# Kernel tuning notes

Hardware: AMD Instinct MI355X
Metric: run time of the kernel (lower is better)

Reference implementation:

```python
import jax, jax.numpy as jnp
import numpy as np

B, S, E, H = 8, 1024, 256, 8
HD = E // H
SCALE = HD ** -0.5
EPS = 1e-5


def setup_inputs() -> dict:
    key = jax.random.key(0)
    ks = jax.random.split(key, 12)
    n = lambda i, shape, sc=1.0: jax.random.normal(ks[i], shape, jnp.float32) * sc
    return {
        "x": n(0, (B, S, E)),
        "x2": n(1, (B, S, E)),
        "pde_qk": n(2, (S, S), 0.1),
        "in_proj_w": n(3, (3 * E, E), 0.03),
        "in_proj_b": jnp.zeros((3 * E,), jnp.float32),
        "out_w": n(4, (E, E), 0.03),
        "out_b": jnp.zeros((E,), jnp.float32),
        "gamma": jnp.ones((E,), jnp.float32),
        "beta": jnp.zeros((E,), jnp.float32),
        "gamma2": jnp.ones((E,), jnp.float32),
        "beta2": jnp.zeros((E,), jnp.float32),
        "bn_weight": jnp.zeros((), jnp.float32),
    }


def _mha(x, pde_qk, wi, bi, wo, bo):
    # qkv in one projection, as in _in_proj with qkv_same
    qkv = x @ wi.T + bi                       # [B,S,3E]
    q, k, v = jnp.split(qkv, 3, axis=-1)
    q = q * SCALE
    hd = lambda t: t.reshape(B, S, H, HD).transpose(0, 2, 1, 3)  # [B,H,S,HD]
    q, k, v = hd(q), hd(k), hd(v)
    # pairwise pde bias fused into scores (broadcast over batch/head)
    scores = jnp.einsum("bhsd,bhtd->bhst", q, k) + pde_qk        # [B,H,S,S]
    w = jax.nn.softmax(scores, axis=-1)
    a = jnp.einsum("bhst,bhtd->bhsd", w, v)
    a = a.transpose(0, 2, 1, 3).reshape(B, S, E)
    return a @ wo.T + bo


def _dual_bn(X, X2, gamma, beta, gamma2, beta2, bn_weight):
    # training branch: learned sigmoid gate mixes per-feature stats across domains
    w = (jax.nn.sigmoid(bn_weight) + 1.0) / 2.0
    m1 = X.mean(axis=(0, 1), keepdims=True)
    v1 = ((X - m1) ** 2).mean(axis=(0, 1), keepdims=True)
    m2 = X2.mean(axis=(0, 1), keepdims=True)
    v2 = ((X2 - m2) ** 2).mean(axis=(0, 1), keepdims=True)
    m_fa = w * m1 + (1 - w) * m2
    m_fb = w * m2 + (1 - w) * m1
    v_fa = w * v1 + (1 - w) * v2
    v_fb = w * v2 + (1 - w) * v1
    Y = gamma * ((X - m_fa) / jnp.sqrt(v_fa + EPS)) + beta
    Y2 = gamma2 * ((X2 - m_fb) / jnp.sqrt(v_fb + EPS)) + beta2
    return Y, Y2


def _mmd(src, tgt, kernel_mul=2.0, kernel_num=5):
    n = src.shape[0] + tgt.shape[0]
    total = jnp.concatenate([src, tgt], axis=0)        # [2B,E]
    d = ((total[None, :, :] - total[:, None, :]) ** 2).sum(-1)  # [2B,2B]
    # bandwidth uses .data (no grad) in torch -> stop_gradient
    bw = jax.lax.stop_gradient(d.sum()) / (n * n - n)
    bw = bw / (kernel_mul ** (kernel_num // 2))
    kern = sum(jnp.exp(-d / (bw * kernel_mul ** i)) for i in range(kernel_num))
    b = src.shape[0]
    XX, YY = kern[:b, :b], kern[b:, b:]
    XY, YX = kern[:b, b:], kern[b:, :b]
    return jnp.mean(XX + YY - XY - YX)


def reference(x, x2, pde_qk, in_proj_w, in_proj_b, out_w, out_b,
              gamma, beta, gamma2, beta2, bn_weight):
    Ya = _mha(x, pde_qk, in_proj_w, in_proj_b, out_w, out_b)
    Yb = _mha(x2, pde_qk, in_proj_w, in_proj_b, out_w, out_b)
    Y, Y2 = _dual_bn(Ya, Yb, gamma, beta, gamma2, beta2, bn_weight)
    # MMD alignment between temporally mean-pooled domain features
    loss = _mmd(Y.mean(axis=1), Y2.mean(axis=1))
    return Y, Y2, loss
```

## Files before the change

### kernel.cpp

```cpp
#include <hip/hip_runtime.h>
#include <hip/hip_bf16.h>

#define B_ 8
#define S_ 1024
#define E_ 256
#define H_ 8
#define HD_ 32
#define SCALE_ 0.17677669529663687f
#define LOG2E_ 1.44269504088896f
#define QSCALE_ (SCALE_ * LOG2E_)
#define EPS_ 1e-5f

typedef __attribute__((ext_vector_type(8))) short bf16x8;
typedef __attribute__((ext_vector_type(4))) short bf16x4;
typedef __attribute__((ext_vector_type(4))) float f32x4;

__device__ inline short f2bf(float f) {
    union { float f; unsigned u; } v; v.f = f;
    unsigned r = v.u + 0x7fff + ((v.u >> 16) & 1);
    return (short)(r >> 16);
}

__device__ inline unsigned packbf(float a, float b) {
    union { float f; unsigned u; } va, vb; va.f = a; vb.f = b;
    return ((va.u + 0x8000u) >> 16) | ((vb.u + 0x8000u) & 0xffff0000u);
}

__device__ inline int swz(int row, int kbyte) {
    return row * 512 + (kbyte ^ ((row & 7) << 4));
}

__global__ __launch_bounds__(256) void k_pde(
    const float* __restrict__ pde, short* __restrict__ out)
{
    int idx = blockIdx.x * 256 + threadIdx.x;
    int s = idx >> 10, t = idx & 1023;
    int dest = (s >> 4) * 16384 + (t >> 4) * 256
             + ((((t >> 2) & 3) << 4) | (s & 15)) * 4 + (t & 3);
    out[dest] = f2bf(pde[idx] * LOG2E_);
}

__global__ __launch_bounds__(256) void k_qkv(
    const float* __restrict__ x0, const float* __restrict__ x1,
    const float* __restrict__ w, const float* __restrict__ bias,
    short* __restrict__ qws, short* __restrict__ kws, short* __restrict__ vws)
{
    __shared__ alignas(16) short lA[64 * 256];
    __shared__ alignas(16) short lB[64 * 256];
    const int m0 = blockIdx.x * 64;
    const int n0 = blockIdx.y * 64;
    const int inp = blockIdx.z;
    const float* x = inp ? x1 : x0;
    const int tid = threadIdx.x;

    #pragma unroll
    for (int i = 0; i < 16; ++i) {
        int fid = tid + 256 * i;
        int r = fid >> 6, c4 = fid & 63;
        float4 vv = *reinterpret_cast<const float4*>(x + (long)(m0 + r) * 256 + c4 * 4);
        short4 sv; sv.x = f2bf(vv.x); sv.y = f2bf(vv.y); sv.z = f2bf(vv.z); sv.w = f2bf(vv.w);
        *reinterpret_cast<short4*>(reinterpret_cast<char*>(lA) + swz(r, c4 * 8)) = sv;
    }
    #pragma unroll
    for (int i = 0; i < 16; ++i) {
        int fid = tid + 256 * i;
        int r = fid >> 6, c4 = fid & 63;
        float4 vv = *reinterpret_cast<const float4*>(w + (long)(n0 + r) * 256 + c4 * 4);
        short4 sv; sv.x = f2bf(vv.x); sv.y = f2bf(vv.y); sv.z = f2bf(vv.z); sv.w = f2bf(vv.w);
        *reinterpret_cast<short4*>(reinterpret_cast<char*>(lB) + swz(r, c4 * 8)) = sv;
    }
    __syncthreads();

    const int wv = tid >> 6, ln = tid & 63;
    const int row16 = ln & 15, kg = ln >> 4;
    const int arow = wv * 16 + row16;
    f32x4 acc[4] = {};
    #pragma unroll
    for (int kc = 0; kc < 8; ++kc) {
        int kbyte = kc * 64 + kg * 16;
        bf16x8 af = *reinterpret_cast<const bf16x8*>(
            reinterpret_cast<char*>(lA) + swz(arow, kbyte));
        #pragma unroll
        for (int n = 0; n < 4; ++n) {
            int brow = n * 16 + row16;
            bf16x8 bfg = *reinterpret_cast<const bf16x8*>(
                reinterpret_cast<char*>(lB) + swz(brow, kbyte));
            acc[n] = __builtin_amdgcn_mfma_f32_16x16x32_bf16(af, bfg, acc[n], 0, 0, 0);
        }
    }
    #pragma unroll
    for (int n = 0; n < 4; ++n) {
        int o = n0 + n * 16 + row16;
        float bval = bias[o];
        int sect = o >> 8, e = o & 255, h = e >> 5, d = e & 31;
        #pragma unroll
        for (int r = 0; r < 4; ++r) {
            int grow = m0 + wv * 16 + kg * 4 + r;
            int b = grow >> 10, s = grow & 1023;
            float val = acc[n][r] + bval;
            long gi = (long)(inp * 64 + b * 8 + h) * 32768;
            if (sect == 0) {
                qws[gi + (s >> 4) * 512 + (((d >> 3) << 4) | (s & 15)) * 8 + (d & 7)]
                    = f2bf(val * QSCALE_);
            } else if (sect == 1) {
                kws[gi + (s >> 4) * 512 + (((d >> 3) << 4) | (s & 15)) * 8 + (d & 7)]
                    = f2bf(val);
            } else {
                vws[gi + (s >> 4) * 512 + (d >> 4) * 256
                       + ((((s >> 2) & 3) << 4) | (d & 15)) * 4 + (s & 3)]
                    = f2bf(val);
            }
        }
    }
}

__global__ __launch_bounds__(256) void k_attn(
    const short* __restrict__ qws, const short* __restrict__ kws,
    const short* __restrict__ vws, const short* __restrict__ pdef,
    short* __restrict__ aout)
{
    const int L = blockIdx.x;
    const int xcd = L & 7, kidx = L >> 3;
    const int qb = kidx >> 4;
    const int g  = xcd * 16 + (kidx & 15);
    const int inp = g >> 6, bh = g & 63, b = bh >> 3, h = bh & 7;
    const int tid = threadIdx.x, wv = tid >> 6, ln = tid & 63;
    const int row16 = ln & 15, kg = ln >> 4;
    const long gbase = (long)g * 32768;
    const int sb = qb * 4 + wv;

    bf16x8 qf = *reinterpret_cast<const bf16x8*>(qws + gbase + sb * 512 + ln * 8);
    const short* kp = kws + gbase + ln * 8;
    const short* vp = vws + gbase + ln * 4;
    const short* pp = pdef + (long)sb * 16384 + ln * 4;

    f32x4 acc0 = {}, acc1 = {};
    float lsum = 0.f;

    #pragma unroll 4
    for (int tb = 0; tb < 64; ++tb) {
        bf16x8 kf = *reinterpret_cast<const bf16x8*>(kp + tb * 512);
        short4 pb = *reinterpret_cast<const short4*>(pp + tb * 256);
        f32x4 c;
        c[0] = __uint_as_float((unsigned)(unsigned short)pb.x << 16);
        c[1] = __uint_as_float((unsigned)(unsigned short)pb.y << 16);
        c[2] = __uint_as_float((unsigned)(unsigned short)pb.z << 16);
        c[3] = __uint_as_float((unsigned)(unsigned short)pb.w << 16);
        f32x4 sv = __builtin_amdgcn_mfma_f32_16x16x32_bf16(kf, qf, c, 0, 0, 0);
        float p0 = exp2f(sv[0]), p1 = exp2f(sv[1]);
        float p2 = exp2f(sv[2]), p3 = exp2f(sv[3]);
        lsum += (p0 + p1) + (p2 + p3);
        union { unsigned u[2]; bf16x4 v; } pa;
        pa.u[0] = packbf(p0, p1);
        pa.u[1] = packbf(p2, p3);
        bf16x4 v0 = *reinterpret_cast<const bf16x4*>(vp + tb * 512);
        bf16x4 v1 = *reinterpret_cast<const bf16x4*>(vp + tb * 512 + 256);
        acc0 = __builtin_amdgcn_mfma_f32_16x16x16bf16_1k(pa.v, v0, acc0, 0, 0, 0);
        acc1 = __builtin_amdgcn_mfma_f32_16x16x16bf16_1k(pa.v, v1, acc1, 0, 0, 0);
    }

    lsum += __shfl_xor(lsum, 16);
    lsum += __shfl_xor(lsum, 32);
    float lq[4];
    #pragma unroll
    for (int r = 0; r < 4; ++r) lq[r] = __shfl(lsum, kg * 4 + r);

    #pragma unroll
    for (int c2 = 0; c2 < 2; ++c2) {
        int e = h * 32 + c2 * 16 + row16;
        #pragma unroll
        for (int r = 0; r < 4; ++r) {
            int s = qb * 64 + wv * 16 + kg * 4 + r;
            float val = (c2 ? acc1[r] : acc0[r]) / lq[r];
            aout[((long)inp * 8192 + b * 1024 + s) * 256 + e] = f2bf(val);
        }
    }
}

__global__ __launch_bounds__(256) void k_outproj(
    const short* __restrict__ a, const float* __restrict__ w,
    const float* __restrict__ bias, float* __restrict__ yout,
    float* __restrict__ chsum, float* __restrict__ chsq,
    float* __restrict__ bsum)
{
    __shared__ alignas(16) short lA[64 * 256];
    __shared__ alignas(16) short lB[64 * 256];
    const int m0 = blockIdx.x * 64;
    const int n0 = blockIdx.y * 64;
    const int inp = blockIdx.z;
    const int tid = threadIdx.x;
    const short* asrc = a + (long)inp * 8192 * 256;

    #pragma unroll
    for (int i = 0; i < 16; ++i) {
        int fid = tid + 256 * i;
        int r = fid >> 6, c4 = fid & 63;
        short4 sv = *reinterpret_cast<const short4*>(asrc + (long)(m0 + r) * 256 + c4 * 4);
        *reinterpret_cast<short4*>(reinterpret_cast<char*>(lA) + swz(r, c4 * 8)) = sv;
    }
    #pragma unroll
    for (int i = 0; i < 16; ++i) {
        int fid = tid + 256 * i;
        int r = fid >> 6, c4 = fid & 63;
        float4 vv = *reinterpret_cast<const float4*>(w + (long)(n0 + r) * 256 + c4 * 4);
        short4 sv; sv.x = f2bf(vv.x); sv.y = f2bf(vv.y); sv.z = f2bf(vv.z); sv.w = f2bf(vv.w);
        *reinterpret_cast<short4*>(reinterpret_cast<char*>(lB) + swz(r, c4 * 8)) = sv;
    }
    __syncthreads();

    const int wv = tid >> 6, ln = tid & 63;
    const int row16 = ln & 15, kg = ln >> 4;
    const int arow = wv * 16 + row16;
    f32x4 acc[4] = {};
    #pragma unroll
    for (int kc = 0; kc < 8; ++kc) {
        int kbyte = kc * 64 + kg * 16;
        bf16x8 af = *reinterpret_cast<const bf16x8*>(
            reinterpret_cast<char*>(lA) + swz(arow, kbyte));
        #pragma unroll
        for (int n = 0; n < 4; ++n) {
            int brow = n * 16 + row16;
            bf16x8 bfg = *reinterpret_cast<const bf16x8*>(
                reinterpret_cast<char*>(lB) + swz(brow, kbyte));
            acc[n] = __builtin_amdgcn_mfma_f32_16x16x32_bf16(af, bfg, acc[n], 0, 0, 0);
        }
    }
    #pragma unroll
    for (int n = 0; n < 4; ++n) {
        int o = n0 + n * 16 + row16;
        float bv = bias[o];
        float sum = 0.f, sq = 0.f;
        #pragma unroll
        for (int r = 0; r < 4; ++r) {
            long grow = m0 + wv * 16 + kg * 4 + r;
            float val = acc[n][r] + bv;
            yout[(long)inp * 2097152 + grow * 256 + o] = val;
            sum += val; sq += val * val;
        }
        sum += __shfl_xor(sum, 16); sum += __shfl_xor(sum, 32);
        sq  += __shfl_xor(sq, 16);  sq  += __shfl_xor(sq, 32);
        if (kg == 0) {
            atomicAdd(&chsum[inp * 256 + o], sum);
            atomicAdd(&chsq[inp * 256 + o], sq);
            int b = m0 >> 10;
            atomicAdd(&bsum[(inp * 8 + b) * 256 + o], sum);
        }
    }
}

__global__ __launch_bounds__(256) void k_finalize(
    const float* __restrict__ chsum, const float* __restrict__ chsq,
    const float* __restrict__ bsum, const float* __restrict__ gamma,
    const float* __restrict__ beta, const float* __restrict__ gamma2,
    const float* __restrict__ beta2, const float* __restrict__ bnw,
    float* __restrict__ params, float* __restrict__ loss_out)
{
    __shared__ float tot[16][257];
    __shared__ float red[8];
    const int tid = threadIdx.x;
    const float w = (1.f / (1.f + __expf(-bnw[0])) + 1.f) * 0.5f;
    const int e = tid;
    float m1 = chsum[e] * (1.f / 8192.f);
    float v1 = chsq[e] * (1.f / 8192.f) - m1 * m1;
    float m2 = chsum[256 + e] * (1.f / 8192.f);
    float v2 = chsq[256 + e] * (1.f / 8192.f) - m2 * m2;
    float mfa = w * m1 + (1.f - w) * m2, mfb = w * m2 + (1.f - w) * m1;
    float vfa = w * v1 + (1.f - w) * v2, vfb = w * v2 + (1.f - w) * v1;
    float sA = gamma[e] * rsqrtf(vfa + EPS_);
    float bA = beta[e] - sA * mfa;
    float sB = gamma2[e] * rsqrtf(vfb + EPS_);
    float bB = beta2[e] - sB * mfb;
    params[e] = sA; params[256 + e] = bA; params[512 + e] = sB; params[768 + e] = bB;
    #pragma unroll
    for (int b = 0; b < 8; ++b) {
        tot[b][e]     = sA * (bsum[b * 256 + e] * (1.f / 1024.f)) + bA;
        tot[8 + b][e] = sB * (bsum[(8 + b) * 256 + e] * (1.f / 1024.f)) + bB;
    }
    __syncthreads();
    const int i = tid >> 4, j = tid & 15;
    float d = 0.f;
    for (int ee = 0; ee < 256; ++ee) {
        float df = tot[i][ee] - tot[j][ee];
        d += df * df;
    }
    float t = d;
    #pragma unroll
    for (int off = 1; off < 64; off <<= 1) t += __shfl_xor(t, off);
    if ((tid & 63) == 0) red[tid >> 6] = t;
    __syncthreads();
    float dsum = red[0] + red[1] + red[2] + red[3];
    float bw = dsum * (1.f / 240.f) * 0.25f;
    float kern = 0.f, bwi = bw;
    #pragma unroll
    for (int kkk = 0; kkk < 5; ++kkk) { kern += __expf(-d / bwi); bwi *= 2.f; }
    float c = (((i < 8) == (j < 8)) ? 1.f : -1.f) * kern;
    #pragma unroll
    for (int off = 1; off < 64; off <<= 1) c += __shfl_xor(c, off);
    if ((tid & 63) == 0) red[4 + (tid >> 6)] = c;
    __syncthreads();
    if (tid == 0) loss_out[0] = (red[4] + red[5] + red[6] + red[7]) * (1.f / 64.f);
}

__global__ __launch_bounds__(256) void k_affine(
    float* __restrict__ y, const float* __restrict__ params)
{
    const long total4 = 4194304 / 4;
    for (long idx4 = (long)blockIdx.x * 256 + threadIdx.x; idx4 < total4;
         idx4 += (long)gridDim.x * 256) {
        long idx = idx4 * 4;
        int inp = (int)((idx >> 21) & 1);
        int e = (int)(idx & 255);
        const float* sA = params + inp * 512;
        const float* bA = sA + 256;
        float4 v = *reinterpret_cast<float4*>(y + idx);
        v.x = sA[e] * v.x + bA[e];
        v.y = sA[e + 1] * v.y + bA[e + 1];
        v.z = sA[e + 2] * v.z + bA[e + 2];
        v.w = sA[e + 3] * v.w + bA[e + 3];
        *reinterpret_cast<float4*>(y + idx) = v;
    }
}

extern "C" void kernel_launch(void* const* d_in, const int* in_sizes, int n_in,
                              void* d_out, int out_size, void* d_ws, size_t ws_size,
                              hipStream_t stream) {
    (void)in_sizes; (void)n_in; (void)out_size; (void)ws_size;
    const float* x    = (const float*)d_in[0];
    const float* x2   = (const float*)d_in[1];
    const float* pde  = (const float*)d_in[2];
    const float* wi   = (const float*)d_in[3];
    const float* bi   = (const float*)d_in[4];
    const float* wo   = (const float*)d_in[5];
    const float* bo   = (const float*)d_in[6];
    const float* gam  = (const float*)d_in[7];
    const float* bet  = (const float*)d_in[8];
    const float* gam2 = (const float*)d_in[9];
    const float* bet2 = (const float*)d_in[10];
    const float* bnw  = (const float*)d_in[11];

    char* ws = (char*)d_ws;
    short* qws = (short*)ws;
    short* kws = (short*)(ws + (8 << 20));
    short* vws = (short*)(ws + (16 << 20));
    short* a   = (short*)(ws + (24 << 20));
    short* pdef = (short*)(ws + (32 << 20));
    float* stats = (float*)(ws + (34 << 20));
    float* chsum = stats;
    float* chsq  = stats + 512;
    float* bsum  = stats + 1024;
    float* params = stats + 1024 + 4096;
    float* y = (float*)d_out;

    hipMemsetAsync(stats, 0, (512 + 512 + 4096) * sizeof(float), stream);
    k_pde<<<4096, 256, 0, stream>>>(pde, pdef);
    k_qkv<<<dim3(128, 12, 2), 256, 0, stream>>>(x, x2, wi, bi, qws, kws, vws);
    k_attn<<<2048, 256, 0, stream>>>(qws, kws, vws, pdef, a);
    k_outproj<<<dim3(128, 4, 2), 256, 0, stream>>>(a, wo, bo, y, chsum, chsq, bsum);
    k_finalize<<<1, 256, 0, stream>>>(chsum, chsq, bsum, gam, bet, gam2, bet2, bnw,
                                      params, y + 4194304);
    k_affine<<<2048, 256, 0, stream>>>(y, params);
}
```

Measured before the change: 153.5 us.

## Pre-convert inputs and weights to bf16 once, keep pde bias in fp32, MFMA row sums

A single grid-stride prep kernel converts x, x2, in_proj and out_proj weights to bf16 once, and writes the pde bias in fp32 with the attention tile layout. This stops every QKV/outproj block from re-reading and re-converting fp32 weights and activations, and lets those kernels load 16-byte bf16 chunks. Attention now loads the bias as fp32 directly, which doubles bias traffic but drops the unpacking. The softmax denominator moves from scalar adds plus shuffles to an extra MFMA against a ones vector. The cost is an extra bf16 copy of x written and read back through the workspace, and the softmax row sums now come from bf16-rounded probabilities.

```diff
diff --git a/kernel.cpp b/kernel.cpp
--- a/kernel.cpp
+++ b/kernel.cpp
@@ -30,19 +30,53 @@
     return row * 512 + (kbyte ^ ((row & 7) << 4));
 }
 
-__global__ __launch_bounds__(256) void k_pde(
-    const float* __restrict__ pde, short* __restrict__ out)
-{
-    int idx = blockIdx.x * 256 + threadIdx.x;
-    int s = idx >> 10, t = idx & 1023;
-    int dest = (s >> 4) * 16384 + (t >> 4) * 256
-             + ((((t >> 2) & 3) << 4) | (s & 15)) * 4 + (t & 3);
-    out[dest] = f2bf(pde[idx] * LOG2E_);
+__global__ __launch_bounds__(256) void k_prep(
+    const float* __restrict__ x0, const float* __restrict__ x1,
+    const float* __restrict__ wi, const float* __restrict__ wo,
+    const float* __restrict__ pde,
+    short* __restrict__ xb, short* __restrict__ wib, short* __restrict__ wob,
+    float* __restrict__ pdef)
+{
+    const int NX  = 2 * 8192 * 256 / 4;
+    const int NWI = 768 * 256 / 4;
+    const int NWO = 256 * 256 / 4;
+    const int NP  = 1024 * 1024 / 4;
+    const int total = NX + NWI + NWO + NP;
+    for (int q4 = blockIdx.x * 256 + threadIdx.x; q4 < total;
+         q4 += gridDim.x * 256) {
+        if (q4 < NX) {
+            long i = (long)q4 * 4;
+            const float* src = (i < 2097152) ? (x0 + i) : (x1 + (i - 2097152));
+            float4 v = *reinterpret_cast<const float4*>(src);
+            short4 s; s.x = f2bf(v.x); s.y = f2bf(v.y); s.z = f2bf(v.z); s.w = f2bf(v.w);
+            *reinterpret_cast<short4*>(xb + i) = s;
+        } else if (q4 < NX + NWI) {
+            long i = (long)(q4 - NX) * 4;
+            float4 v = *reinterpret_cast<const float4*>(wi + i);
+            short4 s; s.x = f2bf(v.x); s.y = f2bf(v.y); s.z = f2bf(v.z); s.w = f2bf(v.w);
+            *reinterpret_cast<short4*>(wib + i) = s;
+        } else if (q4 < NX + NWI + NWO) {
+            long i = (long)(q4 - NX - NWI) * 4;
+            float4 v = *reinterpret_cast<const float4*>(wo + i);
+            short4 s; s.x = f2bf(v.x); s.y = f2bf(v.y); s.z = f2bf(v.z); s.w = f2bf(v.w);
+            *reinterpret_cast<short4*>(wob + i) = s;
+        } else {
+            long i = (long)(q4 - NX - NWI - NWO) * 4;
+            int s = (int)(i >> 10), t = (int)(i & 1023);
+            float4 v = *reinterpret_cast<const float4*>(pde + i);
+            int dest = (s >> 4) * 16384 + (t >> 4) * 256
+                     + ((((t >> 2) & 3) << 4) | (s & 15)) * 4;
+            float4* d = reinterpret_cast<float4*>(pdef + dest);
+            float4 o; o.x = v.x * LOG2E_; o.y = v.y * LOG2E_;
+            o.z = v.z * LOG2E_; o.w = v.w * LOG2E_;
+            *d = o;
+        }
+    }
 }
 
 __global__ __launch_bounds__(256) void k_qkv(
-    const float* __restrict__ x0, const float* __restrict__ x1,
-    const float* __restrict__ w, const float* __restrict__ bias,
+    const short* __restrict__ xb, const short* __restrict__ wib,
+    const float* __restrict__ bias,
     short* __restrict__ qws, short* __restrict__ kws, short* __restrict__ vws)
 {
     __shared__ alignas(16) short lA[64 * 256];
@@ -50,24 +84,22 @@
     const int m0 = blockIdx.x * 64;
     const int n0 = blockIdx.y * 64;
     const int inp = blockIdx.z;
-    const float* x = inp ? x1 : x0;
+    const short* xsrc = xb + (long)inp * 2097152;
     const int tid = threadIdx.x;
 
     #pragma unroll
-    for (int i = 0; i < 16; ++i) {
+    for (int i = 0; i < 8; ++i) {
         int fid = tid + 256 * i;
-        int r = fid >> 6, c4 = fid & 63;
-        float4 vv = *reinterpret_cast<const float4*>(x + (long)(m0 + r) * 256 + c4 * 4);
-        short4 sv; sv.x = f2bf(vv.x); sv.y = f2bf(vv.y); sv.z = f2bf(vv.z); sv.w = f2bf(vv.w);
-        *reinterpret_cast<short4*>(reinterpret_cast<char*>(lA) + swz(r, c4 * 8)) = sv;
-    }
-    #pragma unroll
-    for (int i = 0; i < 16; ++i) {
+        int r = fid >> 5, c = fid & 31;
+        int4 v = *reinterpret_cast<const int4*>(xsrc + (long)(m0 + r) * 256 + c * 8);
+        *reinterpret_cast<int4*>(reinterpret_cast<char*>(lA) + swz(r, c * 16)) = v;
+    }
+    #pragma unroll
+    for (int i = 0; i < 8; ++i) {
         int fid = tid + 256 * i;
-        int r = fid >> 6, c4 = fid & 63;
-        float4 vv = *reinterpret_cast<const float4*>(w + (long)(n0 + r) * 256 + c4 * 4);
-        short4 sv; sv.x = f2bf(vv.x); sv.y = f2bf(vv.y); sv.z = f2bf(vv.z); sv.w = f2bf(vv.w);
-        *reinterpret_cast<short4*>(reinterpret_cast<char*>(lB) + swz(r, c4 * 8)) = sv;
+        int r = fid >> 5, c = fid & 31;
+        int4 v = *reinterpret_cast<const int4*>(wib + (long)(n0 + r) * 256 + c * 8);
+        *reinterpret_cast<int4*>(reinterpret_cast<char*>(lB) + swz(r, c * 16)) = v;
     }
     __syncthreads();
 
@@ -116,7 +148,7 @@
 
 __global__ __launch_bounds__(256) void k_attn(
     const short* __restrict__ qws, const short* __restrict__ kws,
-    const short* __restrict__ vws, const short* __restrict__ pdef,
+    const short* __restrict__ vws, const float* __restrict__ pdef,
     short* __restrict__ aout)
 {
     const int L = blockIdx.x;
@@ -132,24 +164,20 @@
     bf16x8 qf = *reinterpret_cast<const bf16x8*>(qws + gbase + sb * 512 + ln * 8);
     const short* kp = kws + gbase + ln * 8;
     const short* vp = vws + gbase + ln * 4;
-    const short* pp = pdef + (long)sb * 16384 + ln * 4;
-
-    f32x4 acc0 = {}, acc1 = {};
-    float lsum = 0.f;
+    const float* pp = pdef + (long)sb * 16384 + ln * 4;
+
+    union { unsigned u[2]; bf16x4 v; } ones;
+    ones.u[0] = 0x3F803F80u; ones.u[1] = 0x3F803F80u;
+
+    f32x4 acc0 = {}, acc1 = {}, accs = {};
 
     #pragma unroll 4
     for (int tb = 0; tb < 64; ++tb) {
         bf16x8 kf = *reinterpret_cast<const bf16x8*>(kp + tb * 512);
-        short4 pb = *reinterpret_cast<const short4*>(pp + tb * 256);
-        f32x4 c;
-        c[0] = __uint_as_float((unsigned)(unsigned short)pb.x << 16);
-        c[1] = __uint_as_float((unsigned)(unsigned short)pb.y << 16);
-        c[2] = __uint_as_float((unsigned)(unsigned short)pb.z << 16);
-        c[3] = __uint_as_float((unsigned)(unsigned short)pb.w << 16);
+        f32x4 c = *reinterpret_cast<const f32x4*>(pp + tb * 256);
         f32x4 sv = __builtin_amdgcn_mfma_f32_16x16x32_bf16(kf, qf, c, 0, 0, 0);
         float p0 = exp2f(sv[0]), p1 = exp2f(sv[1]);
         float p2 = exp2f(sv[2]), p3 = exp2f(sv[3]);
-        lsum += (p0 + p1) + (p2 + p3);
         union { unsigned u[2]; bf16x4 v; } pa;
         pa.u[0] = packbf(p0, p1);
         pa.u[1] = packbf(p2, p3);
@@ -157,13 +185,8 @@
         bf16x4 v1 = *reinterpret_cast<const bf16x4*>(vp + tb * 512 + 256);
         acc0 = __builtin_amdgcn_mfma_f32_16x16x16bf16_1k(pa.v, v0, acc0, 0, 0, 0);
         acc1 = __builtin_amdgcn_mfma_f32_16x16x16bf16_1k(pa.v, v1, acc1, 0, 0, 0);
-    }
-
-    lsum += __shfl_xor(lsum, 16);
-    lsum += __shfl_xor(lsum, 32);
-    float lq[4];
-    #pragma unroll
-    for (int r = 0; r < 4; ++r) lq[r] = __shfl(lsum, kg * 4 + r);
+        accs = __builtin_amdgcn_mfma_f32_16x16x16bf16_1k(pa.v, ones.v, accs, 0, 0, 0);
+    }
 
     #pragma unroll
     for (int c2 = 0; c2 < 2; ++c2) {
@@ -171,14 +194,14 @@
         #pragma unroll
         for (int r = 0; r < 4; ++r) {
             int s = qb * 64 + wv * 16 + kg * 4 + r;
-            float val = (c2 ? acc1[r] : acc0[r]) / lq[r];
+            float val = (c2 ? acc1[r] : acc0[r]) / accs[r];
             aout[((long)inp * 8192 + b * 1024 + s) * 256 + e] = f2bf(val);
         }
     }
 }
 
 __global__ __launch_bounds__(256) void k_outproj(
-    const short* __restrict__ a, const float* __restrict__ w,
+    const short* __restrict__ a, const short* __restrict__ wob,
     const float* __restrict__ bias, float* __restrict__ yout,
     float* __restrict__ chsum, float* __restrict__ chsq,
     float* __restrict__ bsum)
@@ -192,19 +215,18 @@
     const short* asrc = a + (long)inp * 8192 * 256;
 
     #pragma unroll
-    for (int i = 0; i < 16; ++i) {
+    for (int i = 0; i < 8; ++i) {
         int fid = tid + 256 * i;
-        int r = fid >> 6, c4 = fid & 63;
-        short4 sv = *reinterpret_cast<const short4*>(asrc + (long)(m0 + r) * 256 + c4 * 4);
-        *reinterpret_cast<short4*>(reinterpret_cast<char*>(lA) + swz(r, c4 * 8)) = sv;
-    }
-    #pragma unroll
-    for (int i = 0; i < 16; ++i) {
+        int r = fid >> 5, c = fid & 31;
+        int4 v = *reinterpret_cast<const int4*>(asrc + (long)(m0 + r) * 256 + c * 8);
+        *reinterpret_cast<int4*>(reinterpret_cast<char*>(lA) + swz(r, c * 16)) = v;
+    }
+    #pragma unroll
+    for (int i = 0; i < 8; ++i) {
         int fid = tid + 256 * i;
-        int r = fid >> 6, c4 = fid & 63;
-        float4 vv = *reinterpret_cast<const float4*>(w + (long)(n0 + r) * 256 + c4 * 4);
-        short4 sv; sv.x = f2bf(vv.x); sv.y = f2bf(vv.y); sv.z = f2bf(vv.z); sv.w = f2bf(vv.w);
-        *reinterpret_cast<short4*>(reinterpret_cast<char*>(lB) + swz(r, c4 * 8)) = sv;
+        int r = fid >> 5, c = fid & 31;
+        int4 v = *reinterpret_cast<const int4*>(wob + (long)(n0 + r) * 256 + c * 8);
+        *reinterpret_cast<int4*>(reinterpret_cast<char*>(lB) + swz(r, c * 16)) = v;
     }
     __syncthreads();
 
@@ -339,12 +361,15 @@
     const float* bnw  = (const float*)d_in[11];
 
     char* ws = (char*)d_ws;
-    short* qws = (short*)ws;
-    short* kws = (short*)(ws + (8 << 20));
-    short* vws = (short*)(ws + (16 << 20));
-    short* a   = (short*)(ws + (24 << 20));
-    short* pdef = (short*)(ws + (32 << 20));
-    float* stats = (float*)(ws + (34 << 20));
+    short* xb  = (short*)ws;
+    short* a   = xb;
+    short* qws = (short*)(ws + (8 << 20));
+    short* kws = (short*)(ws + (16 << 20));
+    short* vws = (short*)(ws + (24 << 20));
+    float* pdef = (float*)(ws + (32 << 20));
+    short* wib = (short*)(ws + (36 << 20));
+    short* wob = (short*)(ws + (36 << 20) + (512 << 10));
+    float* stats = (float*)(ws + (37 << 20));
     float* chsum = stats;
     float* chsq  = stats + 512;
     float* bsum  = stats + 1024;
@@ -352,10 +377,10 @@
     float* y = (float*)d_out;
 
     hipMemsetAsync(stats, 0, (512 + 512 + 4096) * sizeof(float), stream);
-    k_pde<<<4096, 256, 0, stream>>>(pde, pdef);
-    k_qkv<<<dim3(128, 12, 2), 256, 0, stream>>>(x, x2, wi, bi, qws, kws, vws);
+    k_prep<<<2048, 256, 0, stream>>>(x, x2, wi, wo, pde, xb, wib, wob, pdef);
+    k_qkv<<<dim3(128, 12, 2), 256, 0, stream>>>(xb, wib, bi, qws, kws, vws);
     k_attn<<<2048, 256, 0, stream>>>(qws, kws, vws, pdef, a);
-    k_outproj<<<dim3(128, 4, 2), 256, 0, stream>>>(a, wo, bo, y, chsum, chsq, bsum);
+    k_outproj<<<dim3(128, 4, 2), 256, 0, stream>>>(a, wob, bo, y, chsum, chsq, bsum);
     k_finalize<<<1, 256, 0, stream>>>(chsum, chsq, bsum, gam, bet, gam2, bet2, bnw,
                                       params, y + 4194304);
     k_affine<<<2048, 256, 0, stream>>>(y, params);
```

After: 148.9 us. 3.0% less time.
